# Kernel optimization log

Hardware: AMD Instinct MI355X
Metric: run time of the kernel (lower is better)

## Reference

```python
import jax, jax.numpy as jnp
import numpy as np

N = 100000; D = 256; ATT = 512; H = 8; HD = ATT // H; E = 250000
TYPE_CT = 64; TS = 64; P = 8192; PC = 1024; MP = 131072; MC = 16384


def setup_inputs() -> dict:
    key = jax.random.key(0)
    ks = jax.random.split(key, 24)
    sD = 1.0 / np.sqrt(D); sT = 1.0 / np.sqrt(TS); sA = 1.0 / np.sqrt(ATT); sC = 1.0 / np.sqrt(D + ATT)
    inp = {}
    inp['node_states'] = jax.random.normal(ks[0], (N, D), jnp.float32)
    inp['node_types'] = jax.random.randint(ks[1], (N,), 0, TYPE_CT, jnp.int32)
    inp['pair_conj'] = jax.random.randint(ks[2], (E,), 0, N, jnp.int32)
    inp['pair_prem'] = jax.random.randint(ks[3], (E,), 0, N, jnp.int32)
    inp['pool_prem_nodes'] = jax.random.randint(ks[4], (MP,), 0, N, jnp.int32)
    inp['pool_prem_seg'] = ((jnp.arange(MP, dtype=jnp.int32) * P) // MP).astype(jnp.int32)  # every prem set non-empty
    inp['pool_conj_nodes'] = jax.random.randint(ks[5], (MC,), 0, N, jnp.int32)
    inp['pool_conj_seg'] = ((jnp.arange(MC, dtype=jnp.int32) * PC) // MC).astype(jnp.int32)
    inp['prem2conj'] = jax.random.randint(ks[6], (P,), 0, PC, jnp.int32)
    # learned parameters
    inp['ln_g'] = jnp.ones((D,), jnp.float32)
    inp['ln_b'] = jnp.zeros((D,), jnp.float32)
    inp['emb_p'] = jax.random.normal(ks[7], (TYPE_CT, TS), jnp.float32) * 0.02
    inp['wp_w'] = jax.random.normal(ks[8], (TS, ATT), jnp.float32) * sT
    inp['wp_b'] = jnp.zeros((ATT,), jnp.float32)
    inp['emb_c'] = jax.random.normal(ks[9], (TYPE_CT, TS), jnp.float32) * 0.02
    inp['wc_w'] = jax.random.normal(ks[10], (TS, ATT), jnp.float32) * sT
    inp['wc_b'] = jnp.zeros((ATT,), jnp.float32)
    inp['Wq_p'] = jax.random.normal(ks[11], (H, D, HD), jnp.float32) * sD
    inp['Wk_p'] = jax.random.normal(ks[12], (H, D, HD), jnp.float32) * sD
    inp['Wv_p'] = jax.random.normal(ks[13], (H, D, HD), jnp.float32) * sD
    inp['Wo_p'] = jax.random.normal(ks[14], (ATT, ATT), jnp.float32) * sA
    inp['Wq_c'] = jax.random.normal(ks[15], (H, D, HD), jnp.float32) * sD
    inp['Wk_c'] = jax.random.normal(ks[16], (H, D, HD), jnp.float32) * sD
    inp['Wv_c'] = jax.random.normal(ks[17], (H, D, HD), jnp.float32) * sD
    inp['Wo_c'] = jax.random.normal(ks[18], (ATT, ATT), jnp.float32) * sA
    inp['W_dag'] = jax.random.normal(ks[19], (D + ATT, D + ATT), jnp.float32) * sC
    inp['b_dag'] = jnp.zeros((D + ATT,), jnp.float32)
    return inp


def _layernorm(x, g, b):
    mu = jnp.mean(x, axis=-1, keepdims=True)
    var = jnp.mean(jnp.square(x - mu), axis=-1, keepdims=True)
    return (x - mu) * jax.lax.rsqrt(var + 1e-5) * g + b


def _mha_dir(x, src, tgt, Wq, Wk, Wv, Wo, gate):
    # gather query/key/value node reprs along the pair list (irregular gather)
    xs = x[src]; xt = x[tgt]                       # [E, D]
    q = jnp.einsum('ed,hdk->ehk', xs, Wq)          # [E, H, HD]
    k = jnp.einsum('ed,hdk->ehk', xt, Wk)
    scores = jnp.sum(q * k, axis=-1) / np.sqrt(HD)  # [E, H]
    # per-query-node (segment) softmax, as in compute_att_aggr grouping
    m = jax.ops.segment_max(scores, src, num_segments=N)
    ex = jnp.exp(scores - m[src])
    denom = jax.ops.segment_sum(ex, src, num_segments=N)
    prob = ex / denom[src]
    v = jnp.einsum('ed,hdk->ehk', xt, Wv)
    # adj_matr @ comb_matr scatter-aggregation
    agg = jax.ops.segment_sum(prob[..., None] * v, src, num_segments=N)  # [N, H, HD]
    return gate * (agg.reshape(N, H * HD) @ Wo)


def reference(node_states, node_types, pair_conj, pair_prem, pool_prem_nodes, pool_prem_seg,
              pool_conj_nodes, pool_conj_seg, prem2conj,
              ln_g, ln_b, emb_p, wp_w, wp_b, emb_c, wc_w, wc_b,
              Wq_p, Wk_p, Wv_p, Wo_p, Wq_c, Wk_c, Wv_c, Wo_c, W_dag, b_dag):
    x = _layernorm(node_states, ln_g, ln_b)                                  # ne_norm(node reprs)
    gate_p = jax.nn.sigmoid(emb_p[node_types] @ wp_w + wp_b)                 # prem_gate  [N, ATT]
    gate_c = jax.nn.sigmoid(emb_c[node_types] @ wc_w + wc_b)                 # conj_gate
    # just_prem pairs: (prem, conj) -> query/scatter node = prem, key/value node = conj
    comb = _mha_dir(x, pair_prem, pair_conj, Wq_p, Wk_p, Wv_p, Wo_p, gate_p)
    # just_conj pairs: (conj, prem)
    comb = comb + _mha_dir(x, pair_conj, pair_prem, Wq_c, Wk_c, Wv_c, Wo_c, gate_c)
    h = jnp.concatenate([x, comb], axis=1)                                   # [N, D+ATT]
    pooled = jnp.tanh(h @ W_dag + b_dag)                                     # simplified dag_lstm pass
    prem_r = jax.ops.segment_max(pooled[pool_prem_nodes], pool_prem_seg, num_segments=P)
    conj_sets = jax.ops.segment_max(pooled[pool_conj_nodes], pool_conj_seg, num_segments=PC)
    conj_r = conj_sets[prem2conj]
    return jnp.concatenate([prem_r, conj_r], axis=1)                         # [P, 2*(D+ATT)]
```

## Files before the change

### kernel.cpp

```cpp
#include <hip/hip_runtime.h>
#include <math.h>

#define N_NODES 100000
#define DIM 256
#define ATT 512
#define NH 8
#define HD 64
#define E_PAIRS 250000
#define TYPE_CT 64
#define TS 64
#define P_SEG 8192
#define PC_SEG 1024
#define MP_SZ 131072
#define MC_SZ 16384
#define CD 768

typedef unsigned short u16;
typedef __attribute__((ext_vector_type(8))) short short8v;
typedef __attribute__((ext_vector_type(4))) float floatx4;

__device__ __forceinline__ u16 f2b(float f) {
    unsigned u = __float_as_uint(f);
    return (u16)((u + 0x7FFFu + ((u >> 16) & 1u)) >> 16);
}
__device__ __forceinline__ float b2f(u16 h) {
    return __uint_as_float(((unsigned)h) << 16);
}

template<int N>
__device__ __forceinline__ void waitcnt_vm() {
    asm volatile("s_waitcnt vmcnt(%0)" :: "n"(N) : "memory");
}
__device__ __forceinline__ void barrier_fence() {
    asm volatile("s_barrier" ::: "memory");
    __builtin_amdgcn_sched_barrier(0);
}

__global__ __launch_bounds__(256) void fill_val_k(float* out, int n, float v) {
    int i = blockIdx.x * 256 + threadIdx.x;
    if (i < n) out[i] = v;
}

__global__ __launch_bounds__(64) void layernorm_k(
    const float* __restrict__ ns, const float* __restrict__ g,
    const float* __restrict__ b, u16* __restrict__ x)
{
    int row = blockIdx.x;
    int lane = threadIdx.x;
    float4 v = ((const float4*)(ns + (size_t)row * DIM))[lane];
    float sum = v.x + v.y + v.z + v.w;
    #pragma unroll
    for (int off = 32; off >= 1; off >>= 1) sum += __shfl_xor(sum, off);
    float mu = sum * (1.0f / DIM);
    float dx = v.x - mu, dy = v.y - mu, dz = v.z - mu, dw = v.w - mu;
    float sq = dx * dx + dy * dy + dz * dz + dw * dw;
    #pragma unroll
    for (int off = 32; off >= 1; off >>= 1) sq += __shfl_xor(sq, off);
    float rs = rsqrtf(sq * (1.0f / DIM) + 1e-5f);
    float4 gg = ((const float4*)g)[lane];
    float4 bb = ((const float4*)b)[lane];
    u16 o4[4];
    o4[0] = f2b(dx * rs * gg.x + bb.x);
    o4[1] = f2b(dy * rs * gg.y + bb.y);
    o4[2] = f2b(dz * rs * gg.z + bb.z);
    o4[3] = f2b(dw * rs * gg.w + bb.w);
    *(uint2*)(x + (size_t)row * DIM + lane * 4) = *(uint2*)o4;
}

__global__ __launch_bounds__(512) void gate_table_k(
    const float* __restrict__ emb, const float* __restrict__ w,
    const float* __restrict__ wb, float* __restrict__ tab)
{
    int t = blockIdx.x;
    int a = threadIdx.x;
    float acc = wb[a];
    #pragma unroll 8
    for (int s = 0; s < TS; ++s) acc += emb[t * TS + s] * w[s * ATT + a];
    tab[t * ATT + a] = 1.0f / (1.0f + expf(-acc));
}

__global__ __launch_bounds__(256) void wcvt_k(
    const float* __restrict__ W, u16* __restrict__ Bt, int K, int N)
{
    int idx = blockIdx.x * 256 + threadIdx.x;
    if (idx >= K * N) return;
    int c = idx / K, k = idx - c * K;
    Bt[idx] = f2b(W[(size_t)k * N + c]);
}

__global__ __launch_bounds__(256) void wqkv_cvt_k(
    const float* __restrict__ Wq, const float* __restrict__ Wk,
    const float* __restrict__ Wv, u16* __restrict__ outp)
{
    int idx = blockIdx.x * 256 + threadIdx.x;
    if (idx >= NH * 3 * HD * DIM) return;
    int k = idx & (DIM - 1);
    int c = (idx >> 8) & (HD - 1);
    int hm = idx >> 14;
    int m = hm % 3;
    int h = hm / 3;
    const float* W = (m == 0) ? Wq : ((m == 1) ? Wk : Wv);
    outp[idx] = f2b(W[((size_t)h * DIM + k) * HD + c]);
}

template<int WN, int EPI>
__device__ __forceinline__ void gemm_body3(
    const u16* __restrict__ A, int lda,
    const u16* __restrict__ A2, int lda2, int K1,
    const u16* __restrict__ Bt, int ldb,
    u16* __restrict__ C, int ldc,
    int M, int K,
    const float* __restrict__ bias,
    const float* __restrict__ gateTab,
    const int* __restrict__ types)
{
    constexpr int BN = 32 * WN;
    constexpr int BR = BN / 64;
    constexpr int LA = 2 + BR;
    __shared__ u16 As[3][128 * 32];
    __shared__ u16 Bs[3][BN * 32];
    const int bm = blockIdx.y * 128;
    const int bn = blockIdx.x * BN;
    const int tid = threadIdx.x;
    const int wave = tid >> 6, lane = tid & 63;
    const int wm = (wave >> 1) * 64, wn = (wave & 1) * 16 * WN;
    const int srow = tid >> 2;
    const int skk = (tid & 3) * 8;
    floatx4 acc[4][WN] = {};

    auto stage = [&](int buf, int k0) {
        #pragma unroll
        for (int rnd = 0; rnd < 2; ++rnd) {
            int grow = bm + srow + rnd * 64;
            if (grow > M - 1) grow = M - 1;
            int gk = k0 + skk;
            const u16* src;
            if (EPI == 2 && gk >= K1) src = A2 + (size_t)grow * lda2 + (gk - K1);
            else                      src = A + (size_t)grow * lda + gk;
            __builtin_amdgcn_global_load_lds(
                (const __attribute__((address_space(1))) void*)src,
                (__attribute__((address_space(3))) void*)(&As[buf][rnd * 2048 + wave * 512]),
                16, 0, 0);
        }
        #pragma unroll
        for (int rnd = 0; rnd < BR; ++rnd) {
            const u16* src = Bt + (size_t)(bn + srow + rnd * 64) * ldb + k0 + skk;
            __builtin_amdgcn_global_load_lds(
                (const __attribute__((address_space(1))) void*)src,
                (__attribute__((address_space(3))) void*)(&Bs[buf][rnd * 2048 + wave * 512]),
                16, 0, 0);
        }
    };

    const int NS = K >> 5;
    stage(0, 0);
    stage(1, 32);
    const int rr = lane & 15, kq = (lane >> 4) * 8;
    int cur = 0;
    for (int is = 0; is < NS; ++is) {
        if (is == NS - 1) waitcnt_vm<0>();
        else              waitcnt_vm<LA>();
        barrier_fence();
        if (is + 2 < NS) stage((cur + 2) % 3, (is + 2) * 32);
        short8v a[4], b[WN];
        #pragma unroll
        for (int i = 0; i < 4; ++i)
            a[i] = *(const short8v*)&As[cur][(wm + i * 16 + rr) * 32 + kq];
        #pragma unroll
        for (int j = 0; j < WN; ++j)
            b[j] = *(const short8v*)&Bs[cur][(wn + j * 16 + rr) * 32 + kq];
        #pragma unroll
        for (int i = 0; i < 4; ++i)
            #pragma unroll
            for (int j = 0; j < WN; ++j)
                acc[i][j] = __builtin_amdgcn_mfma_f32_16x16x32_bf16(
                    a[i], b[j], acc[i][j], 0, 0, 0);
        cur = (cur + 1) % 3;
    }
    #pragma unroll
    for (int i = 0; i < 4; ++i) {
        #pragma unroll
        for (int j = 0; j < WN; ++j) {
            #pragma unroll
            for (int q = 0; q < 4; ++q) {
                int row = bm + wm + i * 16 + (lane >> 4) * 4 + q;
                if (row >= M) continue;
                int col = bn + wn + j * 16 + (lane & 15);
                float v = acc[i][j][q];
                size_t idx = (size_t)row * ldc + col;
                if (EPI == 0) C[idx] = f2b(v);
                else if (EPI == 1) {
                    float g = gateTab[types[row] * ATT + col];
                    C[idx] = f2b(b2f(C[idx]) + g * v);
                } else if (EPI == 3) {
                    float g = gateTab[types[row] * ATT + col];
                    C[idx] = f2b(g * v);
                } else {
                    C[idx] = f2b(tanhf(v + bias[col]));
                }
            }
        }
    }
}

__global__ __launch_bounds__(256) void gemm_qkv(
    const u16* __restrict__ A, const u16* __restrict__ Bt, u16* __restrict__ C)
{
    gemm_body3<6, 0>(A, DIM, nullptr, 0, 1 << 30, Bt, DIM, C, 192,
                     N_NODES, DIM, nullptr, nullptr, nullptr);
}
__global__ __launch_bounds__(256) void gemm_wo_first(
    const u16* __restrict__ A, const u16* __restrict__ Bt, u16* __restrict__ C,
    const float* __restrict__ gateTab, const int* __restrict__ types)
{
    gemm_body3<4, 3>(A, ATT, nullptr, 0, 1 << 30, Bt, ATT, C, ATT,
                     N_NODES, ATT, nullptr, gateTab, types);
}
__global__ __launch_bounds__(256) void gemm_wo_acc(
    const u16* __restrict__ A, const u16* __restrict__ Bt, u16* __restrict__ C,
    const float* __restrict__ gateTab, const int* __restrict__ types)
{
    gemm_body3<4, 1>(A, ATT, nullptr, 0, 1 << 30, Bt, ATT, C, ATT,
                     N_NODES, ATT, nullptr, gateTab, types);
}
__global__ __launch_bounds__(256) void gemm_dag(
    const u16* __restrict__ A, const u16* __restrict__ A2,
    const u16* __restrict__ Bt, u16* __restrict__ C,
    const float* __restrict__ bias)
{
    gemm_body3<4, 2>(A, DIM, A2, ATT, DIM, Bt, CD, C, 384,
                     N_NODES, CD, bias, nullptr, nullptr);
}

__global__ __launch_bounds__(256) void count_k(
    const int* __restrict__ src, int* __restrict__ counts)
{
    int e = blockIdx.x * 256 + threadIdx.x;
    if (e < E_PAIRS) atomicAdd(&counts[src[e]], 1);
}
__global__ __launch_bounds__(256) void scan1_k(
    const int* __restrict__ counts, int* __restrict__ offs, int* __restrict__ bsums)
{
    __shared__ int sm[256];
    int i = blockIdx.x * 256 + threadIdx.x;
    int v = (i < N_NODES) ? counts[i] : 0;
    sm[threadIdx.x] = v;
    __syncthreads();
    for (int d = 1; d < 256; d <<= 1) {
        int t = (threadIdx.x >= d) ? sm[threadIdx.x - d] : 0;
        __syncthreads();
        sm[threadIdx.x] += t;
        __syncthreads();
    }
    if (i < N_NODES) offs[i] = sm[threadIdx.x] - v;
    if (threadIdx.x == 255) bsums[blockIdx.x] = sm[255];
}
__global__ __launch_bounds__(512) void scan2_k(int* __restrict__ bsums, int nb)
{
    __shared__ int sm[512];
    int tx = threadIdx.x;
    int v = (tx < nb) ? bsums[tx] : 0;
    sm[tx] = v;
    __syncthreads();
    for (int d = 1; d < 512; d <<= 1) {
        int t = (tx >= d) ? sm[tx - d] : 0;
        __syncthreads();
        sm[tx] += t;
        __syncthreads();
    }
    if (tx < nb) bsums[tx] = sm[tx] - v;
}
__global__ __launch_bounds__(256) void addcur_k(
    int* __restrict__ offs, const int* __restrict__ bsums, int* __restrict__ cur)
{
    int i = blockIdx.x * 256 + threadIdx.x;
    if (i >= N_NODES) return;
    int o = offs[i] + bsums[i >> 8];
    offs[i] = o;
    cur[i] = o;
}
__global__ __launch_bounds__(256) void scatter_k(
    const int* __restrict__ src, const int* __restrict__ tgt,
    int* __restrict__ cur, int* __restrict__ csr_tgt)
{
    int e = blockIdx.x * 256 + threadIdx.x;
    if (e >= E_PAIRS) return;
    int p = atomicAdd(&cur[src[e]], 1);
    csr_tgt[p] = tgt[e];
}

__global__ __launch_bounds__(256) void attn_k(
    const u16* __restrict__ qkv, const int* __restrict__ offs,
    const int* __restrict__ counts, const int* __restrict__ csr_tgt,
    u16* __restrict__ agg, int h)
{
    int s = blockIdx.x * 4 + (threadIdx.x >> 6);
    if (s >= N_NODES) return;
    int lane = threadIdx.x & 63;
    float q = b2f(qkv[(size_t)s * 192 + lane]) * 0.125f;
    int lo = offs[s], deg = counts[s];
    float m = -INFINITY, l = 0.0f, acc = 0.0f;
    for (int i = 0; i < deg; ++i) {
        int t = csr_tgt[lo + i];
        float kd = b2f(qkv[(size_t)t * 192 + 64 + lane]);
        float vd = b2f(qkv[(size_t)t * 192 + 128 + lane]);
        float p = q * kd;
        #pragma unroll
        for (int off = 32; off >= 1; off >>= 1) p += __shfl_xor(p, off);
        float mn = fmaxf(m, p);
        float sc = expf(m - mn);
        float w  = expf(p - mn);
        l = l * sc + w;
        acc = acc * sc + w * vd;
        m = mn;
    }
    float r = (deg > 0) ? acc / l : 0.0f;
    agg[(size_t)s * ATT + h * HD + lane] = f2b(r);
}

template<int BFOUT>
__global__ __launch_bounds__(256) void seg_max_k(
    const u16* __restrict__ pooled, const int* __restrict__ nodes,
    const int* __restrict__ seg, int total, void* __restrict__ outv, int ldo)
{
    int p = blockIdx.x;
    int lo, hi;
    { int a = 0, b2 = total; while (a < b2) { int mid = (a + b2) >> 1; if (seg[mid] < p) a = mid + 1; else b2 = mid; } lo = a; }
    { int a = lo, b2 = total; while (a < b2) { int mid = (a + b2) >> 1; if (seg[mid] < p + 1) a = mid + 1; else b2 = mid; } hi = a; }
    for (int c = threadIdx.x; c < 384; c += 256) {
        float mx = -INFINITY;
        for (int i = lo; i < hi; ++i)
            mx = fmaxf(mx, b2f(pooled[(size_t)nodes[i] * 384 + c]));
        if (BFOUT) ((u16*)outv)[(size_t)p * ldo + c] = f2b(mx);
        else       ((float*)outv)[(size_t)p * ldo + c] = mx;
    }
}

__global__ __launch_bounds__(768) void gather_conj(
    const u16* __restrict__ cs, const int* __restrict__ p2c,
    float* __restrict__ out)
{
    int p = blockIdx.x;
    int c = threadIdx.x;
    out[(size_t)p * (2 * CD) + CD + c] = b2f(cs[(size_t)p2c[p] * CD + c]);
}

extern "C" void kernel_launch(void* const* d_in, const int* in_sizes, int n_in,
                              void* d_out, int out_size, void* d_ws, size_t ws_size,
                              hipStream_t stream) {
    const float* node_states     = (const float*)d_in[0];
    const int*   node_types      = (const int*)d_in[1];
    const int*   pair_conj       = (const int*)d_in[2];
    const int*   pair_prem       = (const int*)d_in[3];
    const int*   pool_prem_nodes = (const int*)d_in[4];
    const int*   pool_prem_seg   = (const int*)d_in[5];
    const int*   pool_conj_nodes = (const int*)d_in[6];
    const int*   pool_conj_seg   = (const int*)d_in[7];
    const int*   prem2conj       = (const int*)d_in[8];
    const float* ln_g  = (const float*)d_in[9];
    const float* ln_b  = (const float*)d_in[10];
    const float* emb_p = (const float*)d_in[11];
    const float* wp_w  = (const float*)d_in[12];
    const float* wp_b  = (const float*)d_in[13];
    const float* emb_c = (const float*)d_in[14];
    const float* wc_w  = (const float*)d_in[15];
    const float* wc_b  = (const float*)d_in[16];
    const float* Wq_p  = (const float*)d_in[17];
    const float* Wk_p  = (const float*)d_in[18];
    const float* Wv_p  = (const float*)d_in[19];
    const float* Wo_p  = (const float*)d_in[20];
    const float* Wq_c  = (const float*)d_in[21];
    const float* Wk_c  = (const float*)d_in[22];
    const float* Wv_c  = (const float*)d_in[23];
    const float* Wo_c  = (const float*)d_in[24];
    const float* W_dag = (const float*)d_in[25];
    const float* b_dag = (const float*)d_in[26];
    float* out = (float*)d_out;

    char* ws = (char*)d_ws;
    size_t o = 0;
    u16* x_bf  = (u16*)(ws + o); o += (size_t)N_NODES * DIM * 2;
    u16* comb  = (u16*)(ws + o); o += (size_t)N_NODES * ATT * 2;
    u16* R     = (u16*)(ws + o); o += (size_t)N_NODES * ATT * 2;
    char* csrb = ws + o;         o += 8000000;
    u16* conj_sets = (u16*)(ws + o); o += (size_t)PC_SEG * CD * 2;
    const size_t WS_NEEDED = o;

    if (ws_size < WS_NEEDED) {
        fill_val_k<<<(out_size + 255) / 256, 256, 0, stream>>>(out, out_size, (float)ws_size);
        return;
    }

    u16* agg    = R;
    u16* pooled = R;
    int* c_counts[2], *c_offs[2], *c_cur[2], *c_tgt[2];
    for (int d = 0; d < 2; ++d) {
        char* base = csrb + (size_t)d * 2200000;
        c_counts[d] = (int*)(base + 0);
        c_offs[d]   = (int*)(base + 400000);
        c_cur[d]    = (int*)(base + 800000);
        c_tgt[d]    = (int*)(base + 1200000);
    }
    int* bsums = (int*)(csrb + 4400000);
    u16* wdag_t = (u16*)csrb;

    char* ob = (char*)d_out;
    u16* qkv     = (u16*)(ob + 0);
    float* gtab_p = (float*)(ob + 38400000);
    float* gtab_c = (float*)(ob + 38531072);
    u16* wqkv_t  = (u16*)(ob + 38662144);
    u16* wo_t    = (u16*)(ob + 40235008);

    layernorm_k<<<N_NODES, 64, 0, stream>>>(node_states, ln_g, ln_b, x_bf);
    gate_table_k<<<TYPE_CT, ATT, 0, stream>>>(emb_p, wp_w, wp_b, gtab_p);
    gate_table_k<<<TYPE_CT, ATT, 0, stream>>>(emb_c, wc_w, wc_b, gtab_c);
    wqkv_cvt_k<<<(NH * 3 * HD * DIM + 255) / 256, 256, 0, stream>>>(
        Wq_p, Wk_p, Wv_p, wqkv_t);
    wqkv_cvt_k<<<(NH * 3 * HD * DIM + 255) / 256, 256, 0, stream>>>(
        Wq_c, Wk_c, Wv_c, wqkv_t + (size_t)NH * 3 * HD * DIM);
    wcvt_k<<<(ATT * ATT + 255) / 256, 256, 0, stream>>>(Wo_p, wo_t, ATT, ATT);
    wcvt_k<<<(ATT * ATT + 255) / 256, 256, 0, stream>>>(
        Wo_c, wo_t + (size_t)ATT * ATT, ATT, ATT);

    const int NSCAN = (N_NODES + 255) / 256;
    for (int d = 0; d < 2; ++d) {
        const int* src = d ? pair_conj : pair_prem;
        const int* tgt = d ? pair_prem : pair_conj;
        hipMemsetAsync(c_counts[d], 0, 400000, stream);
        count_k<<<(E_PAIRS + 255) / 256, 256, 0, stream>>>(src, c_counts[d]);
        scan1_k<<<NSCAN, 256, 0, stream>>>(c_counts[d], c_offs[d], bsums);
        scan2_k<<<1, 512, 0, stream>>>(bsums, NSCAN);
        addcur_k<<<NSCAN, 256, 0, stream>>>(c_offs[d], bsums, c_cur[d]);
        scatter_k<<<(E_PAIRS + 255) / 256, 256, 0, stream>>>(src, tgt, c_cur[d], c_tgt[d]);
    }

    const int MB128 = (N_NODES + 127) / 128;

    for (int dir = 0; dir < 2; ++dir) {
        const float* gt = dir ? gtab_c : gtab_p;
        const u16* wq_d = wqkv_t + (size_t)dir * NH * 3 * HD * DIM;
        const u16* wo_d = wo_t + (size_t)dir * ATT * ATT;

        for (int h = 0; h < NH; ++h) {
            gemm_qkv<<<dim3(1, MB128), 256, 0, stream>>>(
                x_bf, wq_d + (size_t)h * 3 * HD * DIM, qkv);
            attn_k<<<(N_NODES + 3) / 4, 256, 0, stream>>>(
                qkv, c_offs[dir], c_counts[dir], c_tgt[dir], agg, h);
        }

        if (dir == 0)
            gemm_wo_first<<<dim3(ATT / 128, MB128), 256, 0, stream>>>(
                agg, wo_d, comb, gt, node_types);
        else
            gemm_wo_acc<<<dim3(ATT / 128, MB128), 256, 0, stream>>>(
                agg, wo_d, comb, gt, node_types);
    }

    wcvt_k<<<(CD * CD + 255) / 256, 256, 0, stream>>>(W_dag, wdag_t, CD, CD);

    for (int c0 = 0; c0 < CD; c0 += 384) {
        gemm_dag<<<dim3(3, MB128), 256, 0, stream>>>(
            x_bf, comb, wdag_t + (size_t)c0 * CD, pooled, b_dag + c0);
        seg_max_k<0><<<P_SEG, 256, 0, stream>>>(
            pooled, pool_prem_nodes, pool_prem_seg, MP_SZ, out + c0, 2 * CD);
        seg_max_k<1><<<PC_SEG, 256, 0, stream>>>(
            pooled, pool_conj_nodes, pool_conj_seg, MC_SZ, conj_sets + c0, CD);
    }
    gather_conj<<<P_SEG, CD, 0, stream>>>(conj_sets, prem2conj, out);
}
```

Before: 2.215 ms.

## Switch GEMMs to single-wave 32x64 tiles with swizzled LDS and grouped block order

Replaces the 4-wave 128xBN GEMM blocks with one 64-thread wave computing a 32x64 tile, which removes the block-wide s_barrier. It XOR-swizzles the LDS K offsets to avoid bank conflicts and remaps the flat block index into groups of 8 row tiles for L2 locality. The smaller tiles raise the number of blocks and occupancy but lower data reuse per block and increase A/B traffic. The clamp on out-of-range rows is dropped because N divides evenly by 32.

```diff
diff --git a/kernel.cpp b/kernel.cpp
--- a/kernel.cpp
+++ b/kernel.cpp
@@ -31,9 +31,12 @@
 __device__ __forceinline__ void waitcnt_vm() {
     asm volatile("s_waitcnt vmcnt(%0)" :: "n"(N) : "memory");
 }
-__device__ __forceinline__ void barrier_fence() {
-    asm volatile("s_barrier" ::: "memory");
-    __builtin_amdgcn_sched_barrier(0);
+
+__device__ __forceinline__ void remap8(int flat, int gx, int& bx, int& by) {
+    int yc = flat & 7;
+    int t = flat >> 3;
+    bx = t % gx;
+    by = yc + 8 * (t / gx);
 }
 
 __global__ __launch_bounds__(256) void fill_val_k(float* out, int n, float v) {
@@ -103,8 +106,9 @@
     outp[idx] = f2b(W[((size_t)h * DIM + k) * HD + c]);
 }
 
-template<int WN, int EPI>
-__device__ __forceinline__ void gemm_body3(
+template<int EPI>
+__device__ __forceinline__ void gemm_w(
+    int bm, int bn,
     const u16* __restrict__ A, int lda,
     const u16* __restrict__ A2, int lda2, int K1,
     const u16* __restrict__ Bt, int ldb,
@@ -114,78 +118,76 @@
     const float* __restrict__ gateTab,
     const int* __restrict__ types)
 {
-    constexpr int BN = 32 * WN;
-    constexpr int BR = BN / 64;
-    constexpr int LA = 2 + BR;
-    __shared__ u16 As[3][128 * 32];
-    __shared__ u16 Bs[3][BN * 32];
-    const int bm = blockIdx.y * 128;
-    const int bn = blockIdx.x * BN;
-    const int tid = threadIdx.x;
-    const int wave = tid >> 6, lane = tid & 63;
-    const int wm = (wave >> 1) * 64, wn = (wave & 1) * 16 * WN;
-    const int srow = tid >> 2;
-    const int skk = (tid & 3) * 8;
-    floatx4 acc[4][WN] = {};
+    constexpr int LA = 6;
+    __shared__ u16 As[3][32 * 32];
+    __shared__ u16 Bs[3][64 * 32];
+    const int l = threadIdx.x;
+    const int srow = l >> 2;
+    const int skk = (((l & 3) ^ ((l >> 3) & 3)) * 8);
+    floatx4 acc[2][4] = {};
 
     auto stage = [&](int buf, int k0) {
         #pragma unroll
         for (int rnd = 0; rnd < 2; ++rnd) {
-            int grow = bm + srow + rnd * 64;
-            if (grow > M - 1) grow = M - 1;
+            int grow = bm + srow + rnd * 16;
             int gk = k0 + skk;
             const u16* src;
             if (EPI == 2 && gk >= K1) src = A2 + (size_t)grow * lda2 + (gk - K1);
             else                      src = A + (size_t)grow * lda + gk;
             __builtin_amdgcn_global_load_lds(
                 (const __attribute__((address_space(1))) void*)src,
-                (__attribute__((address_space(3))) void*)(&As[buf][rnd * 2048 + wave * 512]),
+                (__attribute__((address_space(3))) void*)(&As[buf][rnd * 512]),
                 16, 0, 0);
         }
         #pragma unroll
-        for (int rnd = 0; rnd < BR; ++rnd) {
-            const u16* src = Bt + (size_t)(bn + srow + rnd * 64) * ldb + k0 + skk;
+        for (int rnd = 0; rnd < 4; ++rnd) {
+            const u16* src = Bt + (size_t)(bn + srow + rnd * 16) * ldb + k0 + skk;
             __builtin_amdgcn_global_load_lds(
                 (const __attribute__((address_space(1))) void*)src,
-                (__attribute__((address_space(3))) void*)(&Bs[buf][rnd * 2048 + wave * 512]),
+                (__attribute__((address_space(3))) void*)(&Bs[buf][rnd * 512]),
                 16, 0, 0);
         }
     };
 
     const int NS = K >> 5;
     stage(0, 0);
-    stage(1, 32);
-    const int rr = lane & 15, kq = (lane >> 4) * 8;
+    if (NS > 1) stage(1, 32);
+    const int rr = l & 15;
+    const int cq = l >> 4;
     int cur = 0;
     for (int is = 0; is < NS; ++is) {
         if (is == NS - 1) waitcnt_vm<0>();
         else              waitcnt_vm<LA>();
-        barrier_fence();
+        __builtin_amdgcn_sched_barrier(0);
         if (is + 2 < NS) stage((cur + 2) % 3, (is + 2) * 32);
-        short8v a[4], b[WN];
-        #pragma unroll
-        for (int i = 0; i < 4; ++i)
-            a[i] = *(const short8v*)&As[cur][(wm + i * 16 + rr) * 32 + kq];
-        #pragma unroll
-        for (int j = 0; j < WN; ++j)
-            b[j] = *(const short8v*)&Bs[cur][(wn + j * 16 + rr) * 32 + kq];
-        #pragma unroll
-        for (int i = 0; i < 4; ++i)
+        short8v a[2], b[4];
+        #pragma unroll
+        for (int i = 0; i < 2; ++i) {
+            int ar = i * 16 + rr;
+            a[i] = *(const short8v*)&As[cur][ar * 32 + ((cq ^ ((ar >> 1) & 3)) * 8)];
+        }
+        #pragma unroll
+        for (int j = 0; j < 4; ++j) {
+            int br = j * 16 + rr;
+            b[j] = *(const short8v*)&Bs[cur][br * 32 + ((cq ^ ((br >> 1) & 3)) * 8)];
+        }
+        #pragma unroll
+        for (int i = 0; i < 2; ++i)
             #pragma unroll
-            for (int j = 0; j < WN; ++j)
+            for (int j = 0; j < 4; ++j)
                 acc[i][j] = __builtin_amdgcn_mfma_f32_16x16x32_bf16(
                     a[i], b[j], acc[i][j], 0, 0, 0);
         cur = (cur + 1) % 3;
     }
     #pragma unroll
-    for (int i = 0; i < 4; ++i) {
-        #pragma unroll
-        for (int j = 0; j < WN; ++j) {
+    for (int i = 0; i < 2; ++i) {
+        #pragma unroll
+        for (int j = 0; j < 4; ++j) {
             #pragma unroll
             for (int q = 0; q < 4; ++q) {
-                int row = bm + wm + i * 16 + (lane >> 4) * 4 + q;
+                int row = bm + i * 16 + (l >> 4) * 4 + q;
                 if (row >= M) continue;
-                int col = bn + wn + j * 16 + (lane & 15);
+                int col = bn + j * 16 + (l & 15);
                 float v = acc[i][j][q];
                 size_t idx = (size_t)row * ldc + col;
                 if (EPI == 0) C[idx] = f2b(v);
@@ -203,33 +205,44 @@
     }
 }
 
-__global__ __launch_bounds__(256) void gemm_qkv(
+#define MB32 3125
+#define MB32P 3128
+
+__global__ __launch_bounds__(64) void gemm_qkv(
     const u16* __restrict__ A, const u16* __restrict__ Bt, u16* __restrict__ C)
 {
-    gemm_body3<6, 0>(A, DIM, nullptr, 0, 1 << 30, Bt, DIM, C, 192,
-                     N_NODES, DIM, nullptr, nullptr, nullptr);
-}
-__global__ __launch_bounds__(256) void gemm_wo_first(
+    int bx, by; remap8(blockIdx.x, 3, bx, by);
+    if (by >= MB32) return;
+    gemm_w<0>(by * 32, bx * 64, A, DIM, nullptr, 0, 1 << 30, Bt, DIM, C, 192,
+              N_NODES, DIM, nullptr, nullptr, nullptr);
+}
+__global__ __launch_bounds__(64) void gemm_wo_first(
     const u16* __restrict__ A, const u16* __restrict__ Bt, u16* __restrict__ C,
     const float* __restrict__ gateTab, const int* __restrict__ types)
 {
-    gemm_body3<4, 3>(A, ATT, nullptr, 0, 1 << 30, Bt, ATT, C, ATT,
-                     N_NODES, ATT, nullptr, gateTab, types);
-}
-__global__ __launch_bounds__(256) void gemm_wo_acc(
+    int bx, by; remap8(blockIdx.x, 8, bx, by);
+    if (by >= MB32) return;
+    gemm_w<3>(by * 32, bx * 64, A, ATT, nullptr, 0, 1 << 30, Bt, ATT, C, ATT,
+              N_NODES, ATT, nullptr, gateTab, types);
+}
+__global__ __launch_bounds__(64) void gemm_wo_acc(
     const u16* __restrict__ A, const u16* __restrict__ Bt, u16* __restrict__ C,
     const float* __restrict__ gateTab, const int* __restrict__ types)
 {
-    gemm_body3<4, 1>(A, ATT, nullptr, 0, 1 << 30, Bt, ATT, C, ATT,
-                     N_NODES, ATT, nullptr, gateTab, types);
-}
-__global__ __launch_bounds__(256) void gemm_dag(
+    int bx, by; remap8(blockIdx.x, 8, bx, by);
+    if (by >= MB32) return;
+    gemm_w<1>(by * 32, bx * 64, A, ATT, nullptr, 0, 1 << 30, Bt, ATT, C, ATT,
+              N_NODES, ATT, nullptr, gateTab, types);
+}
+__global__ __launch_bounds__(64) void gemm_dag(
     const u16* __restrict__ A, const u16* __restrict__ A2,
     const u16* __restrict__ Bt, u16* __restrict__ C,
     const float* __restrict__ bias)
 {
-    gemm_body3<4, 2>(A, DIM, A2, ATT, DIM, Bt, CD, C, 384,
-                     N_NODES, CD, bias, nullptr, nullptr);
+    int bx, by; remap8(blockIdx.x, 6, bx, by);
+    if (by >= MB32) return;
+    gemm_w<2>(by * 32, bx * 64, A, DIM, A2, ATT, DIM, Bt, CD, C, 384,
+              N_NODES, CD, bias, nullptr, nullptr);
 }
 
 __global__ __launch_bounds__(256) void count_k(
@@ -434,32 +447,30 @@
         scatter_k<<<(E_PAIRS + 255) / 256, 256, 0, stream>>>(src, tgt, c_cur[d], c_tgt[d]);
     }
 
-    const int MB128 = (N_NODES + 127) / 128;
-
     for (int dir = 0; dir < 2; ++dir) {
         const float* gt = dir ? gtab_c : gtab_p;
         const u16* wq_d = wqkv_t + (size_t)dir * NH * 3 * HD * DIM;
         const u16* wo_d = wo_t + (size_t)dir * ATT * ATT;
 
         for (int h = 0; h < NH; ++h) {
-            gemm_qkv<<<dim3(1, MB128), 256, 0, stream>>>(
+            gemm_qkv<<<3 * MB32P, 64, 0, stream>>>(
                 x_bf, wq_d + (size_t)h * 3 * HD * DIM, qkv);
             attn_k<<<(N_NODES + 3) / 4, 256, 0, stream>>>(
                 qkv, c_offs[dir], c_counts[dir], c_tgt[dir], agg, h);
         }
 
         if (dir == 0)
-            gemm_wo_first<<<dim3(ATT / 128, MB128), 256, 0, stream>>>(
+            gemm_wo_first<<<8 * MB32P, 64, 0, stream>>>(
                 agg, wo_d, comb, gt, node_types);
         else
-            gemm_wo_acc<<<dim3(ATT / 128, MB128), 256, 0, stream>>>(
+            gemm_wo_acc<<<8 * MB32P, 64, 0, stream>>>(
                 agg, wo_d, comb, gt, node_types);
     }
 
     wcvt_k<<<(CD * CD + 255) / 256, 256, 0, stream>>>(W_dag, wdag_t, CD, CD);
 
     for (int c0 = 0; c0 < CD; c0 += 384) {
-        gemm_dag<<<dim3(3, MB128), 256, 0, stream>>>(
+        gemm_dag<<<6 * MB32P, 64, 0, stream>>>(
             x_bf, comb, wdag_t + (size_t)c0 * CD, pooled, b_dag + c0);
         seg_max_k<0><<<P_SEG, 256, 0, stream>>>(
             pooled, pool_prem_nodes, pool_prem_seg, MP_SZ, out + c0, 2 * CD);
```

Result: slower. 2.606 ms (+17.7%).
